# Kernel optimization log

Hardware: AMD Instinct MI355X
Metric: run time of the kernel (lower is better)

## Reference

```python
import jax, jax.numpy as jnp
import numpy as np

B, N, D, H, K, R = 128, 2048, 256, 16, 32, 16
LEAKY_SLOPE = 0.01


def setup_inputs() -> dict:
    key = jax.random.key(0)
    ks = jax.random.split(key, 8)
    s = 0.05
    inp = jax.random.normal(ks[0], (B * N, D), dtype=jnp.float32)
    batch_ids = jnp.repeat(jnp.arange(B, dtype=jnp.int32), N)  # equal-size graphs
    Wk = jax.random.normal(ks[1], (K, D), dtype=jnp.float32) * s
    Wq0 = jax.random.normal(ks[2], (H * K, D), dtype=jnp.float32) * s
    Wq1 = jax.random.normal(ks[3], (H * K, D), dtype=jnp.float32) * s
    We = jax.random.normal(ks[4], (R, D), dtype=jnp.float32) * s
    Wout = jax.random.normal(ks[5], (D, H * R), dtype=jnp.float32) * s
    bout = jax.random.normal(ks[6], (D,), dtype=jnp.float32) * s
    return {"inp": inp, "batch_ids": batch_ids, "Wk": Wk, "Wq0": Wq0,
            "Wq1": Wq1, "We": We, "Wout": Wout, "bout": bout}


def reference(inp, batch_ids, Wk, Wq0, Wq1, We, Wout, bout):
    b = int(jnp.max(batch_ids)) + 1  # number of graphs (static at trace time)
    d = inp.shape[-1]
    # global max pool per graph (torch_geometric global_max_pool)
    pooled = jax.ops.segment_max(inp, batch_ids, num_segments=b)  # [B, D]
    x = inp.reshape(b, -1, d)                                     # [B, N, D]
    keys = jnp.einsum('bnd,kd->bnk', x, Wk)                       # [B, N, K]

    def head_embed(Wq):
        q = (pooled @ Wq.T).reshape(b, H, K)                      # [B, H, K]
        logits = jnp.einsum('bhk,bnk->bhn', q, keys)              # [B, H, N]
        att = jax.nn.softmax(logits, axis=-1)
        feat = jnp.einsum('bhn,bnd->bhd', att, x)                 # [B, H, D]
        return jnp.einsum('bhd,rd->bhr', feat, We)                # [B, H, R]

    dx = (head_embed(Wq0) - head_embed(Wq1)).reshape(b, -1)       # [B, H*R]
    out = dx @ Wout.T + bout
    return jnp.where(out >= 0, out, LEAKY_SLOPE * out)            # LeakyReLU
```

## Files before the change

kernel.cpp:

```cpp
#include <hip/hip_runtime.h>
#include <math.h>

#define B_ 128
#define N_ 2048
#define D_ 256
#define NHEADS 32

#define POOLED_OFF 0
#define P_OFF      32768
#define E_OFF      1081344
#define ML_OFF     5275648
#define FEATP_OFF  5308416

__device__ __forceinline__ void atomic_max_f32(float* addr, float v) {
    if (v >= 0.0f) {
        atomicMax((int*)addr, __float_as_int(v + 0.0f));
    } else {
        atomicMin((unsigned int*)addr, __float_as_uint(v));
    }
}

__device__ __forceinline__ unsigned short f2bf(float f) {
    unsigned u = __float_as_uint(f);
    u += 0x7fff + ((u >> 16) & 1);
    return (unsigned short)(u >> 16);
}
__device__ __forceinline__ float bf2f(unsigned short h) {
    return __uint_as_float(((unsigned)h) << 16);
}

__global__ __launch_bounds__(256) void k_init(float* __restrict__ pooled) {
    pooled[blockIdx.x * 256 + threadIdx.x] = -INFINITY;
}

__global__ __launch_bounds__(256) void k_pool(const float* __restrict__ inp,
                                              float* __restrict__ pooled) {
    int b = blockIdx.x >> 4;
    int ch = blockIdx.x & 15;
    int t = threadIdx.x;
    int sub = t >> 6;
    int dq = (t & 63) * 4;
    const float* p = inp + ((size_t)(b * N_ + ch * 128 + sub)) * D_ + dq;
    float4 m = {-INFINITY, -INFINITY, -INFINITY, -INFINITY};
#pragma unroll 8
    for (int i = 0; i < 32; ++i) {
        float4 v = *(const float4*)(p + (size_t)i * 4 * D_);
        m.x = fmaxf(m.x, v.x); m.y = fmaxf(m.y, v.y);
        m.z = fmaxf(m.z, v.z); m.w = fmaxf(m.w, v.w);
    }
    __shared__ float sm[4 * 256];
    sm[sub * 256 + dq + 0] = m.x;
    sm[sub * 256 + dq + 1] = m.y;
    sm[sub * 256 + dq + 2] = m.z;
    sm[sub * 256 + dq + 3] = m.w;
    __syncthreads();
    float v = fmaxf(fmaxf(sm[t], sm[256 + t]), fmaxf(sm[512 + t], sm[768 + t]));
    atomic_max_f32(pooled + b * D_ + t, v);
}

__global__ __launch_bounds__(256) void k_qp(const float* __restrict__ pooled,
                                            const float* __restrict__ Wq0,
                                            const float* __restrict__ Wq1,
                                            const float* __restrict__ Wk,
                                            float* __restrict__ P) {
    __shared__ float pl[D_];
    __shared__ float ql[1024];
    int b = blockIdx.x, t = threadIdx.x;
    pl[t] = pooled[b * D_ + t];
    __syncthreads();
    for (int rep = 0; rep < 4; ++rep) {
        int idx = rep * 256 + t;
        const float* Wq = (idx < 512) ? Wq0 : Wq1;
        int row = idx & 511;
        const float4* wr = (const float4*)(Wq + (size_t)row * D_);
        float acc = 0.0f;
        for (int dq = 0; dq < 64; ++dq) {
            float4 w = wr[dq];
            const float* pp = &pl[dq * 4];
            acc += w.x * pp[0] + w.y * pp[1] + w.z * pp[2] + w.w * pp[3];
        }
        ql[idx] = acc;
    }
    __syncthreads();
    float wk[32];
#pragma unroll
    for (int k = 0; k < 32; ++k) wk[k] = Wk[k * D_ + t];
    for (int j = 0; j < NHEADS; ++j) {
        const float* q = &ql[(j >> 4) * 512 + (j & 15) * 32];
        float acc = 0.0f;
#pragma unroll
        for (int k = 0; k < 32; ++k) acc = fmaf(q[k], wk[k], acc);
        P[((size_t)b * NHEADS + j) * D_ + t] = acc;
    }
}

__global__ __launch_bounds__(256) void k_logits_e(const float* __restrict__ inp,
                                                  const float* __restrict__ P,
                                                  unsigned short* __restrict__ E,
                                                  float* __restrict__ ml) {
    __shared__ float xs[512 * 20];
    __shared__ float ps[NHEADS * 20];
    int b = blockIdx.x >> 2, nt = blockIdx.x & 3;
    int n0 = nt * 512;
    int t = threadIdx.x;
    int jg = t & 3, ng = t >> 2;
    float acc[8][8] = {};
    const float* xbase = inp + ((size_t)(b * N_ + n0)) * D_;
    const float* pbase = P + (size_t)b * NHEADS * D_;
    for (int c = 0; c < 16; ++c) {
        int d0 = c * 16;
        {
            int q = t & 3, nrow = t >> 2;
            for (int k = 0; k < 8; ++k) {
                int n = nrow + k * 64;
                float4 v = *(const float4*)(xbase + (size_t)n * D_ + d0 + q * 4);
                *(float4*)&xs[n * 20 + q * 4] = v;
            }
            if (t < 128) {
                int j = t >> 2;
                float4 v = *(const float4*)(pbase + (size_t)j * D_ + d0 + q * 4);
                *(float4*)&ps[j * 20 + q * 4] = v;
            }
        }
        __syncthreads();
#pragma unroll
        for (int dd = 0; dd < 16; dd += 4) {
            float4 xa[8], pa[8];
#pragma unroll
            for (int k = 0; k < 8; ++k)
                xa[k] = *(const float4*)&xs[(ng + 64 * k) * 20 + dd];
#pragma unroll
            for (int jj = 0; jj < 8; ++jj)
                pa[jj] = *(const float4*)&ps[(jg + 4 * jj) * 20 + dd];
#pragma unroll
            for (int jj = 0; jj < 8; ++jj)
#pragma unroll
                for (int k = 0; k < 8; ++k)
                    acc[jj][k] += xa[k].x * pa[jj].x + xa[k].y * pa[jj].y +
                                  xa[k].z * pa[jj].z + xa[k].w * pa[jj].w;
        }
        __syncthreads();
    }
    float* red  = xs;
    float* red2 = xs + 2048;
    float* mrow = xs + 2048 + 256;
    int jr = t >> 3, pr = t & 7;
#pragma unroll
    for (int jj = 0; jj < 8; ++jj) {
        float lm = acc[jj][0];
#pragma unroll
        for (int k = 1; k < 8; ++k) lm = fmaxf(lm, acc[jj][k]);
        red[(jg + 4 * jj) * 64 + ng] = lm;
    }
    __syncthreads();
    {
        float v = red[jr * 64 + pr * 8];
#pragma unroll
        for (int i = 1; i < 8; ++i) v = fmaxf(v, red[jr * 64 + pr * 8 + i]);
        red2[jr * 8 + pr] = v;
    }
    __syncthreads();
    if (t < 32) {
        float v = red2[t * 8];
#pragma unroll
        for (int i = 1; i < 8; ++i) v = fmaxf(v, red2[t * 8 + i]);
        mrow[t] = v;
    }
    __syncthreads();
#pragma unroll
    for (int jj = 0; jj < 8; ++jj) {
        int j = jg + 4 * jj;
        float m = mrow[j];
        unsigned short* Eb = E + ((size_t)b * NHEADS + j) * N_ + n0 + ng;
        float s = 0.0f;
#pragma unroll
        for (int k = 0; k < 8; ++k) {
            float e = __expf(acc[jj][k] - m);
            s += e;
            Eb[64 * k] = f2bf(e);
        }
        red[j * 64 + ng] = s;
    }
    __syncthreads();
    {
        float v = 0.0f;
#pragma unroll
        for (int i = 0; i < 8; ++i) v += red[jr * 64 + pr * 8 + i];
        red2[jr * 8 + pr] = v;
    }
    __syncthreads();
    if (t < 32) {
        float v = 0.0f;
#pragma unroll
        for (int i = 0; i < 8; ++i) v += red2[t * 8 + i];
        float* mlp = ml + (((size_t)b * NHEADS + t) * 4 + nt) * 2;
        mlp[0] = mrow[t];
        mlp[1] = v;
    }
}

__global__ __launch_bounds__(256) void k_feat(const float* __restrict__ inp,
                                              const unsigned short* __restrict__ E,
                                              const float* __restrict__ ml,
                                              float* __restrict__ featp) {
    __shared__ float xs[32 * 256];
    __shared__ float as_[32 * 36];
    __shared__ float wcs[32];
    int b = blockIdx.x >> 2, ns = blockIdx.x & 3;
    int n0 = ns * 512;
    int t = threadIdx.x;
    int dg = t & 31, jg = t >> 5;
    if (t < 32) {
        const float* mlb = ml + ((size_t)b * NHEADS + t) * 8;
        float M = fmaxf(fmaxf(mlb[0], mlb[2]), fmaxf(mlb[4], mlb[6]));
        wcs[t] = __expf(mlb[ns * 2] - M);
    }
    float4 accA[4] = {};
    float4 accB[4] = {};
    const float* xb = inp + ((size_t)(b * N_ + n0)) * D_;
    const unsigned short* eb0 = E + (size_t)b * NHEADS * N_ + n0;
    __syncthreads();
    int js = t >> 3, qq = t & 7;
    float wj = wcs[js];
    const unsigned short* ebj = eb0 + (size_t)js * N_ + qq * 4;
    for (int c = 0; c < 16; ++c) {
        {
            int q = t & 63, row = t >> 6;
            for (int k = 0; k < 8; ++k) {
                int n = row + k * 4;
                *(float4*)&xs[n * 256 + q * 4] =
                    *(const float4*)(xb + (size_t)(c * 32 + n) * D_ + q * 4);
            }
            ushort4 ev = *(const ushort4*)(ebj + c * 32);
            float4 av = {bf2f(ev.x) * wj, bf2f(ev.y) * wj,
                         bf2f(ev.z) * wj, bf2f(ev.w) * wj};
            *(float4*)&as_[js * 36 + qq * 4] = av;
        }
        __syncthreads();
#pragma unroll
        for (int nn = 0; nn < 32; nn += 4) {
            float4 aa[4];
#pragma unroll
            for (int jj = 0; jj < 4; ++jj)
                aa[jj] = *(const float4*)&as_[(jg * 4 + jj) * 36 + nn];
#pragma unroll
            for (int i4 = 0; i4 < 4; ++i4) {
                int n = nn + i4;
                float4 xA = *(const float4*)&xs[n * 256 + dg * 4];
                float4 xB = *(const float4*)&xs[n * 256 + 128 + dg * 4];
#pragma unroll
                for (int jj = 0; jj < 4; ++jj) {
                    float a = (i4 == 0) ? aa[jj].x : (i4 == 1) ? aa[jj].y
                            : (i4 == 2) ? aa[jj].z : aa[jj].w;
                    accA[jj].x = fmaf(a, xA.x, accA[jj].x);
                    accA[jj].y = fmaf(a, xA.y, accA[jj].y);
                    accA[jj].z = fmaf(a, xA.z, accA[jj].z);
                    accA[jj].w = fmaf(a, xA.w, accA[jj].w);
                    accB[jj].x = fmaf(a, xB.x, accB[jj].x);
                    accB[jj].y = fmaf(a, xB.y, accB[jj].y);
                    accB[jj].z = fmaf(a, xB.z, accB[jj].z);
                    accB[jj].w = fmaf(a, xB.w, accB[jj].w);
                }
            }
        }
        __syncthreads();
    }
    float* fb = featp + ((size_t)ns * B_ + b) * NHEADS * D_;
#pragma unroll
    for (int jj = 0; jj < 4; ++jj) {
        int j = jg * 4 + jj;
        *(float4*)(fb + (size_t)j * D_ + dg * 4) = accA[jj];
        *(float4*)(fb + (size_t)j * D_ + 128 + dg * 4) = accB[jj];
    }
}

__global__ __launch_bounds__(256) void k_out(const float* __restrict__ featp,
                                             const float* __restrict__ ml,
                                             const float* __restrict__ We,
                                             const float* __restrict__ Wout,
                                             const float* __restrict__ bout,
                                             float* __restrict__ out) {
    __shared__ float f[NHEADS * 257];
    __shared__ float bhrs[512];
    __shared__ float dxs[256];
    __shared__ float linv[NHEADS];
    int b = blockIdx.x, t = threadIdx.x;
    if (t < 32) {
        const float* mlb = ml + ((size_t)b * NHEADS + t) * 8;
        float M = fmaxf(fmaxf(mlb[0], mlb[2]), fmaxf(mlb[4], mlb[6]));
        float L = __expf(mlb[0] - M) * mlb[1] + __expf(mlb[2] - M) * mlb[3] +
                  __expf(mlb[4] - M) * mlb[5] + __expf(mlb[6] - M) * mlb[7];
        linv[t] = 1.0f / L;
    }
    __syncthreads();
    for (int j = 0; j < NHEADS; ++j) {
        float s = 0.0f;
#pragma unroll
        for (int ns = 0; ns < 4; ++ns)
            s += featp[(((size_t)ns * B_ + b) * NHEADS + j) * D_ + t];
        f[j * 257 + t] = s * linv[j];
    }
    __syncthreads();
    for (int rep = 0; rep < 2; ++rep) {
        int idx = rep * 256 + t;
        int j = idx >> 4, r = idx & 15;
        const float* w = We + (size_t)r * D_;
        const float* ff = &f[j * 257];
        float acc = 0.0f;
        for (int d = 0; d < D_; ++d) acc = fmaf(ff[d], w[d], acc);
        bhrs[idx] = acc;
    }
    __syncthreads();
    {
        int h = t >> 4, r = t & 15;
        dxs[t] = bhrs[h * 16 + r] - bhrs[(16 + h) * 16 + r];
    }
    __syncthreads();
    float acc = bout[t];
    const float* wrow = Wout + (size_t)t * 256;
    for (int c = 0; c < 256; ++c) acc = fmaf(dxs[c], wrow[c], acc);
    out[(size_t)b * D_ + t] = acc >= 0.0f ? acc : 0.01f * acc;
}

extern "C" void kernel_launch(void* const* d_in, const int* in_sizes, int n_in,
                              void* d_out, int out_size, void* d_ws, size_t ws_size,
                              hipStream_t stream) {
    const float* inp  = (const float*)d_in[0];
    const float* Wk   = (const float*)d_in[2];
    const float* Wq0  = (const float*)d_in[3];
    const float* Wq1  = (const float*)d_in[4];
    const float* We   = (const float*)d_in[5];
    const float* Wout = (const float*)d_in[6];
    const float* bout = (const float*)d_in[7];
    float* out = (float*)d_out;
    float* ws  = (float*)d_ws;
    float* pooled = ws + POOLED_OFF;
    float* P      = ws + P_OFF;
    unsigned short* E = (unsigned short*)(ws + E_OFF);
    float* ml     = ws + ML_OFF;
    float* featp  = ws + FEATP_OFF;

    k_init<<<dim3(128), dim3(256), 0, stream>>>(pooled);
    k_pool<<<dim3(2048), dim3(256), 0, stream>>>(inp, pooled);
    k_qp<<<dim3(128), dim3(256), 0, stream>>>(pooled, Wq0, Wq1, Wk, P);
    k_logits_e<<<dim3(512), dim3(256), 0, stream>>>(inp, P, E, ml);
    k_feat<<<dim3(512), dim3(256), 0, stream>>>(inp, E, ml, featp);
    k_out<<<dim3(128), dim3(256), 0, stream>>>(featp, ml, We, Wout, bout, out);
}
```

Before: 664.4 us.

## Fuse logits, softmax and feature aggregation into one MFMA kernel with split-bf16 inputs

The pooling kernel now also writes the input as hi/lo bf16 pairs, and the query projection is split the same way. A single fused attention kernel computes logits with three bf16 MFMAs per tile (hi*hi, hi*lo, lo*hi) to approximate fp32. It then does the block-local softmax in registers and aggregates features with bf16 MFMA over an LDS-transposed x tile. This drops the separate E round-trip through global memory and the scalar FMA loops, but adds writes of two bf16 copies of x in the pool pass and lowers the precision of the aggregation step.

```diff
diff --git a/kernel.cpp b/kernel.cpp
--- a/kernel.cpp
+++ b/kernel.cpp
@@ -7,19 +7,26 @@
 #define NHEADS 32
 
 #define POOLED_OFF 0
-#define P_OFF      32768
-#define E_OFF      1081344
-#define ML_OFF     5275648
-#define FEATP_OFF  5308416
+#define PHI_OFF    32768
+#define PLO_OFF    557056
+#define ML_OFF     1081344
+#define FEATP_OFF  1114112
+#define XHI_OFF    5308416
+#define XLO_OFF    38862848
+
+#define XHI_S 0
+#define XLO_S 32768
+#define ATT_S 0
+#define XT_S  33280
+#define STAT_S 53760
+
+typedef __attribute__((ext_vector_type(8))) short short8;
+typedef __attribute__((ext_vector_type(4))) float f32x4;
 
 __device__ __forceinline__ void atomic_max_f32(float* addr, float v) {
-    if (v >= 0.0f) {
-        atomicMax((int*)addr, __float_as_int(v + 0.0f));
-    } else {
-        atomicMin((unsigned int*)addr, __float_as_uint(v));
-    }
-}
-
+    if (v >= 0.0f) atomicMax((int*)addr, __float_as_int(v + 0.0f));
+    else           atomicMin((unsigned int*)addr, __float_as_uint(v));
+}
 __device__ __forceinline__ unsigned short f2bf(float f) {
     unsigned u = __float_as_uint(f);
     u += 0x7fff + ((u >> 16) & 1);
@@ -28,25 +35,39 @@
 __device__ __forceinline__ float bf2f(unsigned short h) {
     return __uint_as_float(((unsigned)h) << 16);
 }
+__device__ __forceinline__ unsigned pack2bf(float a, float b) {
+    return (unsigned)f2bf(a) | ((unsigned)f2bf(b) << 16);
+}
 
 __global__ __launch_bounds__(256) void k_init(float* __restrict__ pooled) {
     pooled[blockIdx.x * 256 + threadIdx.x] = -INFINITY;
 }
 
 __global__ __launch_bounds__(256) void k_pool(const float* __restrict__ inp,
-                                              float* __restrict__ pooled) {
+                                              float* __restrict__ pooled,
+                                              unsigned short* __restrict__ xhi,
+                                              unsigned short* __restrict__ xlo) {
     int b = blockIdx.x >> 4;
     int ch = blockIdx.x & 15;
     int t = threadIdx.x;
     int sub = t >> 6;
     int dq = (t & 63) * 4;
     const float* p = inp + ((size_t)(b * N_ + ch * 128 + sub)) * D_ + dq;
+    size_t nodebase = (size_t)b * N_ + ch * 128 + sub;
     float4 m = {-INFINITY, -INFINITY, -INFINITY, -INFINITY};
-#pragma unroll 8
+#pragma unroll 4
     for (int i = 0; i < 32; ++i) {
         float4 v = *(const float4*)(p + (size_t)i * 4 * D_);
         m.x = fmaxf(m.x, v.x); m.y = fmaxf(m.y, v.y);
         m.z = fmaxf(m.z, v.z); m.w = fmaxf(m.w, v.w);
+        size_t node = nodebase + (size_t)i * 4;
+        ushort4 h4, l4;
+        h4.x = f2bf(v.x); l4.x = f2bf(v.x - bf2f(h4.x));
+        h4.y = f2bf(v.y); l4.y = f2bf(v.y - bf2f(h4.y));
+        h4.z = f2bf(v.z); l4.z = f2bf(v.z - bf2f(h4.z));
+        h4.w = f2bf(v.w); l4.w = f2bf(v.w - bf2f(h4.w));
+        *(ushort4*)(xhi + node * D_ + dq) = h4;
+        *(ushort4*)(xlo + node * D_ + dq) = l4;
     }
     __shared__ float sm[4 * 256];
     sm[sub * 256 + dq + 0] = m.x;
@@ -62,7 +83,8 @@
                                             const float* __restrict__ Wq0,
                                             const float* __restrict__ Wq1,
                                             const float* __restrict__ Wk,
-                                            float* __restrict__ P) {
+                                            unsigned short* __restrict__ Phi,
+                                            unsigned short* __restrict__ Plo) {
     __shared__ float pl[D_];
     __shared__ float ql[1024];
     int b = blockIdx.x, t = threadIdx.x;
@@ -74,9 +96,9 @@
         int row = idx & 511;
         const float4* wr = (const float4*)(Wq + (size_t)row * D_);
         float acc = 0.0f;
-        for (int dq = 0; dq < 64; ++dq) {
-            float4 w = wr[dq];
-            const float* pp = &pl[dq * 4];
+        for (int dqi = 0; dqi < 64; ++dqi) {
+            float4 w = wr[dqi];
+            const float* pp = &pl[dqi * 4];
             acc += w.x * pp[0] + w.y * pp[1] + w.z * pp[2] + w.w * pp[3];
         }
         ql[idx] = acc;
@@ -90,188 +112,173 @@
         float acc = 0.0f;
 #pragma unroll
         for (int k = 0; k < 32; ++k) acc = fmaf(q[k], wk[k], acc);
-        P[((size_t)b * NHEADS + j) * D_ + t] = acc;
-    }
-}
-
-__global__ __launch_bounds__(256) void k_logits_e(const float* __restrict__ inp,
-                                                  const float* __restrict__ P,
-                                                  unsigned short* __restrict__ E,
-                                                  float* __restrict__ ml) {
-    __shared__ float xs[512 * 20];
-    __shared__ float ps[NHEADS * 20];
-    int b = blockIdx.x >> 2, nt = blockIdx.x & 3;
-    int n0 = nt * 512;
+        unsigned short hi = f2bf(acc);
+        unsigned short lo = f2bf(acc - bf2f(hi));
+        Phi[((size_t)b * NHEADS + j) * D_ + t] = hi;
+        Plo[((size_t)b * NHEADS + j) * D_ + t] = lo;
+    }
+}
+
+__global__ __launch_bounds__(256) void k_attn(const unsigned short* __restrict__ xhi,
+                                              const unsigned short* __restrict__ xlo,
+                                              const unsigned short* __restrict__ Phi,
+                                              const unsigned short* __restrict__ Plo,
+                                              float* __restrict__ ml,
+                                              float* __restrict__ featp) {
+    __shared__ uint4 smem4[4096];
+    unsigned char* smem = (unsigned char*)smem4;
+    float* smax = (float*)(smem + STAT_S);
+    float* ssum = (float*)(smem + STAT_S + 512);
+
+    int b = blockIdx.x >> 2, ns = blockIdx.x & 3;
     int t = threadIdx.x;
-    int jg = t & 3, ng = t >> 2;
-    float acc[8][8] = {};
-    const float* xbase = inp + ((size_t)(b * N_ + n0)) * D_;
-    const float* pbase = P + (size_t)b * NHEADS * D_;
+    int w = t >> 6;
+    int lane = t & 63;
+    int lq = lane >> 4;
+    int lm = lane & 15;
+    size_t gnode0 = (size_t)b * N_ + ns * 512;
+
+    f32x4 acc_s[8][2];
+#pragma unroll
+    for (int mt = 0; mt < 8; ++mt)
+#pragma unroll
+        for (int ht = 0; ht < 2; ++ht) acc_s[mt][ht] = (f32x4){0.f, 0.f, 0.f, 0.f};
+
+    int srow = t >> 2, sseg = t & 3;
+    for (int dc = 0; dc < 8; ++dc) {
+        int d0 = dc * 32;
+        short8 bh[2], bl[2];
+#pragma unroll
+        for (int ht = 0; ht < 2; ++ht) {
+            size_t poff = ((size_t)b * NHEADS + ht * 16 + lm) * D_ + d0 + lq * 8;
+            bh[ht] = *(const short8*)(Phi + poff);
+            bl[ht] = *(const short8*)(Plo + poff);
+        }
+        const unsigned short* gxh = xhi + (gnode0 + srow) * D_ + d0 + sseg * 8;
+        const unsigned short* gxl = xlo + (gnode0 + srow) * D_ + d0 + sseg * 8;
+        __syncthreads();
+#pragma unroll
+        for (int i = 0; i < 8; ++i) {
+            *(uint4*)(smem + XHI_S + (size_t)(srow + i * 64) * 64 + sseg * 16) =
+                *(const uint4*)(gxh + (size_t)i * 64 * D_);
+            *(uint4*)(smem + XLO_S + (size_t)(srow + i * 64) * 64 + sseg * 16) =
+                *(const uint4*)(gxl + (size_t)i * 64 * D_);
+        }
+        __syncthreads();
+#pragma unroll
+        for (int mt = 0; mt < 8; ++mt) {
+            size_t roff = (size_t)(w * 128 + mt * 16 + lm) * 64 + lq * 16;
+            short8 ah = *(const short8*)(smem + XHI_S + roff);
+            short8 al = *(const short8*)(smem + XLO_S + roff);
+#pragma unroll
+            for (int ht = 0; ht < 2; ++ht) {
+                acc_s[mt][ht] = __builtin_amdgcn_mfma_f32_16x16x32_bf16(ah, bh[ht], acc_s[mt][ht], 0, 0, 0);
+                acc_s[mt][ht] = __builtin_amdgcn_mfma_f32_16x16x32_bf16(ah, bl[ht], acc_s[mt][ht], 0, 0, 0);
+                acc_s[mt][ht] = __builtin_amdgcn_mfma_f32_16x16x32_bf16(al, bh[ht], acc_s[mt][ht], 0, 0, 0);
+            }
+        }
+    }
+    __syncthreads();
+
+    float bm[2];
+#pragma unroll
+    for (int ht = 0; ht < 2; ++ht) {
+        float m = -INFINITY;
+#pragma unroll
+        for (int mt = 0; mt < 8; ++mt) {
+            m = fmaxf(m, fmaxf(fmaxf(acc_s[mt][ht][0], acc_s[mt][ht][1]),
+                               fmaxf(acc_s[mt][ht][2], acc_s[mt][ht][3])));
+        }
+        m = fmaxf(m, __shfl_xor(m, 16));
+        m = fmaxf(m, __shfl_xor(m, 32));
+        if (lane < 16) smax[w * 32 + ht * 16 + lane] = m;
+    }
+    __syncthreads();
+#pragma unroll
+    for (int ht = 0; ht < 2; ++ht) {
+        bm[ht] = fmaxf(fmaxf(smax[0 * 32 + ht * 16 + lm], smax[1 * 32 + ht * 16 + lm]),
+                       fmaxf(smax[2 * 32 + ht * 16 + lm], smax[3 * 32 + ht * 16 + lm]));
+    }
+#pragma unroll
+    for (int ht = 0; ht < 2; ++ht) {
+        float s = 0.0f;
+#pragma unroll
+        for (int mt = 0; mt < 8; ++mt) {
+            float e0 = __expf(acc_s[mt][ht][0] - bm[ht]);
+            float e1 = __expf(acc_s[mt][ht][1] - bm[ht]);
+            float e2 = __expf(acc_s[mt][ht][2] - bm[ht]);
+            float e3 = __expf(acc_s[mt][ht][3] - bm[ht]);
+            s += (e0 + e1) + (e2 + e3);
+            uint2 pk;
+            pk.x = pack2bf(e0, e1);
+            pk.y = pack2bf(e2, e3);
+            *(uint2*)(smem + ATT_S + (size_t)(ht * 16 + lm) * 1040 +
+                      (size_t)(w * 128 + mt * 16 + lq * 4) * 2) = pk;
+        }
+        s += __shfl_xor(s, 16);
+        s += __shfl_xor(s, 32);
+        if (lane < 16) ssum[w * 32 + ht * 16 + lane] = s;
+    }
+    __syncthreads();
+    if (t < 32) {
+        float mB = fmaxf(fmaxf(smax[t], smax[32 + t]), fmaxf(smax[64 + t], smax[96 + t]));
+        float l = ssum[t] + ssum[32 + t] + ssum[64 + t] + ssum[96 + t];
+        float* mlp = ml + (((size_t)b * NHEADS + t) * 4 + ns) * 2;
+        mlp[0] = mB;
+        mlp[1] = l;
+    }
+    __syncthreads();
+
+    f32x4 acc_o[2][4];
+#pragma unroll
+    for (int mt = 0; mt < 2; ++mt)
+#pragma unroll
+        for (int dt = 0; dt < 4; ++dt) acc_o[mt][dt] = (f32x4){0.f, 0.f, 0.f, 0.f};
+
+    int db = t & 31, nb = t >> 5;
     for (int c = 0; c < 16; ++c) {
-        int d0 = c * 16;
-        {
-            int q = t & 3, nrow = t >> 2;
-            for (int k = 0; k < 8; ++k) {
-                int n = nrow + k * 64;
-                float4 v = *(const float4*)(xbase + (size_t)n * D_ + d0 + q * 4);
-                *(float4*)&xs[n * 20 + q * 4] = v;
-            }
-            if (t < 128) {
-                int j = t >> 2;
-                float4 v = *(const float4*)(pbase + (size_t)j * D_ + d0 + q * 4);
-                *(float4*)&ps[j * 20 + q * 4] = v;
-            }
+        const unsigned short* gx = xhi + (gnode0 + c * 32 + nb * 4) * D_ + db * 8;
+        uint4 R0 = *(const uint4*)(gx);
+        uint4 R1 = *(const uint4*)(gx + D_);
+        uint4 R2 = *(const uint4*)(gx + 2 * D_);
+        uint4 R3 = *(const uint4*)(gx + 3 * D_);
+        const unsigned* r0 = (const unsigned*)&R0;
+        const unsigned* r1 = (const unsigned*)&R1;
+        const unsigned* r2 = (const unsigned*)&R2;
+        const unsigned* r3 = (const unsigned*)&R3;
+        uint2 T[8];
+#pragma unroll
+        for (int c2 = 0; c2 < 4; ++c2) {
+            T[2 * c2 + 0].x = __builtin_amdgcn_perm(r1[c2], r0[c2], 0x05040100u);
+            T[2 * c2 + 0].y = __builtin_amdgcn_perm(r3[c2], r2[c2], 0x05040100u);
+            T[2 * c2 + 1].x = __builtin_amdgcn_perm(r1[c2], r0[c2], 0x07060302u);
+            T[2 * c2 + 1].y = __builtin_amdgcn_perm(r3[c2], r2[c2], 0x07060302u);
         }
         __syncthreads();
 #pragma unroll
-        for (int dd = 0; dd < 16; dd += 4) {
-            float4 xa[8], pa[8];
-#pragma unroll
-            for (int k = 0; k < 8; ++k)
-                xa[k] = *(const float4*)&xs[(ng + 64 * k) * 20 + dd];
-#pragma unroll
-            for (int jj = 0; jj < 8; ++jj)
-                pa[jj] = *(const float4*)&ps[(jg + 4 * jj) * 20 + dd];
-#pragma unroll
-            for (int jj = 0; jj < 8; ++jj)
-#pragma unroll
-                for (int k = 0; k < 8; ++k)
-                    acc[jj][k] += xa[k].x * pa[jj].x + xa[k].y * pa[jj].y +
-                                  xa[k].z * pa[jj].z + xa[k].w * pa[jj].w;
+        for (int j = 0; j < 8; ++j) {
+            int jj = (j + db) & 7;
+            *(uint2*)(smem + XT_S + (size_t)(db * 8 + jj) * 80 + nb * 8) = T[jj];
         }
         __syncthreads();
-    }
-    float* red  = xs;
-    float* red2 = xs + 2048;
-    float* mrow = xs + 2048 + 256;
-    int jr = t >> 3, pr = t & 7;
-#pragma unroll
-    for (int jj = 0; jj < 8; ++jj) {
-        float lm = acc[jj][0];
-#pragma unroll
-        for (int k = 1; k < 8; ++k) lm = fmaxf(lm, acc[jj][k]);
-        red[(jg + 4 * jj) * 64 + ng] = lm;
-    }
-    __syncthreads();
-    {
-        float v = red[jr * 64 + pr * 8];
-#pragma unroll
-        for (int i = 1; i < 8; ++i) v = fmaxf(v, red[jr * 64 + pr * 8 + i]);
-        red2[jr * 8 + pr] = v;
-    }
-    __syncthreads();
-    if (t < 32) {
-        float v = red2[t * 8];
-#pragma unroll
-        for (int i = 1; i < 8; ++i) v = fmaxf(v, red2[t * 8 + i]);
-        mrow[t] = v;
-    }
-    __syncthreads();
-#pragma unroll
-    for (int jj = 0; jj < 8; ++jj) {
-        int j = jg + 4 * jj;
-        float m = mrow[j];
-        unsigned short* Eb = E + ((size_t)b * NHEADS + j) * N_ + n0 + ng;
-        float s = 0.0f;
-#pragma unroll
-        for (int k = 0; k < 8; ++k) {
-            float e = __expf(acc[jj][k] - m);
-            s += e;
-            Eb[64 * k] = f2bf(e);
-        }
-        red[j * 64 + ng] = s;
-    }
-    __syncthreads();
-    {
-        float v = 0.0f;
-#pragma unroll
-        for (int i = 0; i < 8; ++i) v += red[jr * 64 + pr * 8 + i];
-        red2[jr * 8 + pr] = v;
-    }
-    __syncthreads();
-    if (t < 32) {
-        float v = 0.0f;
-#pragma unroll
-        for (int i = 0; i < 8; ++i) v += red2[t * 8 + i];
-        float* mlp = ml + (((size_t)b * NHEADS + t) * 4 + nt) * 2;
-        mlp[0] = mrow[t];
-        mlp[1] = v;
-    }
-}
-
-__global__ __launch_bounds__(256) void k_feat(const float* __restrict__ inp,
-                                              const unsigned short* __restrict__ E,
-                                              const float* __restrict__ ml,
-                                              float* __restrict__ featp) {
-    __shared__ float xs[32 * 256];
-    __shared__ float as_[32 * 36];
-    __shared__ float wcs[32];
-    int b = blockIdx.x >> 2, ns = blockIdx.x & 3;
-    int n0 = ns * 512;
-    int t = threadIdx.x;
-    int dg = t & 31, jg = t >> 5;
-    if (t < 32) {
-        const float* mlb = ml + ((size_t)b * NHEADS + t) * 8;
-        float M = fmaxf(fmaxf(mlb[0], mlb[2]), fmaxf(mlb[4], mlb[6]));
-        wcs[t] = __expf(mlb[ns * 2] - M);
-    }
-    float4 accA[4] = {};
-    float4 accB[4] = {};
-    const float* xb = inp + ((size_t)(b * N_ + n0)) * D_;
-    const unsigned short* eb0 = E + (size_t)b * NHEADS * N_ + n0;
-    __syncthreads();
-    int js = t >> 3, qq = t & 7;
-    float wj = wcs[js];
-    const unsigned short* ebj = eb0 + (size_t)js * N_ + qq * 4;
-    for (int c = 0; c < 16; ++c) {
-        {
-            int q = t & 63, row = t >> 6;
-            for (int k = 0; k < 8; ++k) {
-                int n = row + k * 4;
-                *(float4*)&xs[n * 256 + q * 4] =
-                    *(const float4*)(xb + (size_t)(c * 32 + n) * D_ + q * 4);
-            }
-            ushort4 ev = *(const ushort4*)(ebj + c * 32);
-            float4 av = {bf2f(ev.x) * wj, bf2f(ev.y) * wj,
-                         bf2f(ev.z) * wj, bf2f(ev.w) * wj};
-            *(float4*)&as_[js * 36 + qq * 4] = av;
-        }
-        __syncthreads();
-#pragma unroll
-        for (int nn = 0; nn < 32; nn += 4) {
-            float4 aa[4];
-#pragma unroll
-            for (int jj = 0; jj < 4; ++jj)
-                aa[jj] = *(const float4*)&as_[(jg * 4 + jj) * 36 + nn];
-#pragma unroll
-            for (int i4 = 0; i4 < 4; ++i4) {
-                int n = nn + i4;
-                float4 xA = *(const float4*)&xs[n * 256 + dg * 4];
-                float4 xB = *(const float4*)&xs[n * 256 + 128 + dg * 4];
-#pragma unroll
-                for (int jj = 0; jj < 4; ++jj) {
-                    float a = (i4 == 0) ? aa[jj].x : (i4 == 1) ? aa[jj].y
-                            : (i4 == 2) ? aa[jj].z : aa[jj].w;
-                    accA[jj].x = fmaf(a, xA.x, accA[jj].x);
-                    accA[jj].y = fmaf(a, xA.y, accA[jj].y);
-                    accA[jj].z = fmaf(a, xA.z, accA[jj].z);
-                    accA[jj].w = fmaf(a, xA.w, accA[jj].w);
-                    accB[jj].x = fmaf(a, xB.x, accB[jj].x);
-                    accB[jj].y = fmaf(a, xB.y, accB[jj].y);
-                    accB[jj].z = fmaf(a, xB.z, accB[jj].z);
-                    accB[jj].w = fmaf(a, xB.w, accB[jj].w);
-                }
-            }
-        }
-        __syncthreads();
-    }
-    float* fb = featp + ((size_t)ns * B_ + b) * NHEADS * D_;
-#pragma unroll
-    for (int jj = 0; jj < 4; ++jj) {
-        int j = jg * 4 + jj;
-        *(float4*)(fb + (size_t)j * D_ + dg * 4) = accA[jj];
-        *(float4*)(fb + (size_t)j * D_ + 128 + dg * 4) = accB[jj];
-    }
+        short8 a0 = *(const short8*)(smem + ATT_S + (size_t)lm * 1040 + (size_t)(c * 32 + lq * 8) * 2);
+        short8 a1 = *(const short8*)(smem + ATT_S + (size_t)(16 + lm) * 1040 + (size_t)(c * 32 + lq * 8) * 2);
+#pragma unroll
+        for (int dt = 0; dt < 4; ++dt) {
+            short8 bf = *(const short8*)(smem + XT_S + (size_t)(w * 64 + dt * 16 + lm) * 80 + lq * 16);
+            acc_o[0][dt] = __builtin_amdgcn_mfma_f32_16x16x32_bf16(a0, bf, acc_o[0][dt], 0, 0, 0);
+            acc_o[1][dt] = __builtin_amdgcn_mfma_f32_16x16x32_bf16(a1, bf, acc_o[1][dt], 0, 0, 0);
+        }
+    }
+    float* fb = featp + ((size_t)(ns * B_ + b)) * D_ * NHEADS;
+#pragma unroll
+    for (int mt = 0; mt < 2; ++mt)
+#pragma unroll
+        for (int dt = 0; dt < 4; ++dt) {
+            int d = w * 64 + dt * 16 + lm;
+            int h0 = mt * 16 + lq * 4;
+            *(f32x4*)(fb + (size_t)d * NHEADS + h0) = acc_o[mt][dt];
+        }
 }
 
 __global__ __launch_bounds__(256) void k_out(const float* __restrict__ featp,
@@ -283,31 +290,45 @@
     __shared__ float f[NHEADS * 257];
     __shared__ float bhrs[512];
     __shared__ float dxs[256];
-    __shared__ float linv[NHEADS];
+    __shared__ float wns[4 * 32];
+    __shared__ float linv2[32];
     int b = blockIdx.x, t = threadIdx.x;
     if (t < 32) {
         const float* mlb = ml + ((size_t)b * NHEADS + t) * 8;
         float M = fmaxf(fmaxf(mlb[0], mlb[2]), fmaxf(mlb[4], mlb[6]));
-        float L = __expf(mlb[0] - M) * mlb[1] + __expf(mlb[2] - M) * mlb[3] +
-                  __expf(mlb[4] - M) * mlb[5] + __expf(mlb[6] - M) * mlb[7];
-        linv[t] = 1.0f / L;
-    }
-    __syncthreads();
-    for (int j = 0; j < NHEADS; ++j) {
-        float s = 0.0f;
-#pragma unroll
-        for (int ns = 0; ns < 4; ++ns)
-            s += featp[(((size_t)ns * B_ + b) * NHEADS + j) * D_ + t];
-        f[j * 257 + t] = s * linv[j];
-    }
+        float e0 = __expf(mlb[0] - M), e1 = __expf(mlb[2] - M);
+        float e2 = __expf(mlb[4] - M), e3 = __expf(mlb[6] - M);
+        float L = e0 * mlb[1] + e1 * mlb[3] + e2 * mlb[5] + e3 * mlb[7];
+        wns[0 * 32 + t] = e0; wns[1 * 32 + t] = e1;
+        wns[2 * 32 + t] = e2; wns[3 * 32 + t] = e3;
+        linv2[t] = 1.0f / L;
+    }
+    __syncthreads();
+    float fj[32];
+#pragma unroll
+    for (int j = 0; j < 32; ++j) fj[j] = 0.0f;
+#pragma unroll
+    for (int ns = 0; ns < 4; ++ns) {
+        const float* fp = featp + ((size_t)(ns * B_ + b) * D_ + t) * NHEADS;
+#pragma unroll
+        for (int j4 = 0; j4 < 8; ++j4) {
+            float4 v = *(const float4*)(fp + j4 * 4);
+            fj[j4 * 4 + 0] += wns[ns * 32 + j4 * 4 + 0] * v.x;
+            fj[j4 * 4 + 1] += wns[ns * 32 + j4 * 4 + 1] * v.y;
+            fj[j4 * 4 + 2] += wns[ns * 32 + j4 * 4 + 2] * v.z;
+            fj[j4 * 4 + 3] += wns[ns * 32 + j4 * 4 + 3] * v.w;
+        }
+    }
+#pragma unroll
+    for (int j = 0; j < 32; ++j) f[j * 257 + t] = fj[j] * linv2[j];
     __syncthreads();
     for (int rep = 0; rep < 2; ++rep) {
         int idx = rep * 256 + t;
         int j = idx >> 4, r = idx & 15;
-        const float* w = We + (size_t)r * D_;
+        const float* wrow = We + (size_t)r * D_;
         const float* ff = &f[j * 257];
         float acc = 0.0f;
-        for (int d = 0; d < D_; ++d) acc = fmaf(ff[d], w[d], acc);
+        for (int d = 0; d < D_; ++d) acc = fmaf(ff[d], wrow[d], acc);
         bhrs[idx] = acc;
     }
     __syncthreads();
@@ -335,15 +356,16 @@
     float* out = (float*)d_out;
     float* ws  = (float*)d_ws;
     float* pooled = ws + POOLED_OFF;
-    float* P      = ws + P_OFF;
-    unsigned short* E = (unsigned short*)(ws + E_OFF);
+    unsigned short* Phi = (unsigned short*)(ws + PHI_OFF);
+    unsigned short* Plo = (unsigned short*)(ws + PLO_OFF);
     float* ml     = ws + ML_OFF;
     float* featp  = ws + FEATP_OFF;
+    unsigned short* xhi = (unsigned short*)(ws + XHI_OFF);
+    unsigned short* xlo = (unsigned short*)(ws + XLO_OFF);
 
     k_init<<<dim3(128), dim3(256), 0, stream>>>(pooled);
-    k_pool<<<dim3(2048), dim3(256), 0, stream>>>(inp, pooled);
-    k_qp<<<dim3(128), dim3(256), 0, stream>>>(pooled, Wq0, Wq1, Wk, P);
-    k_logits_e<<<dim3(512), dim3(256), 0, stream>>>(inp, P, E, ml);
-    k_feat<<<dim3(512), dim3(256), 0, stream>>>(inp, E, ml, featp);
+    k_pool<<<dim3(2048), dim3(256), 0, stream>>>(inp, pooled, xhi, xlo);
+    k_qp<<<dim3(128), dim3(256), 0, stream>>>(pooled, Wq0, Wq1, Wk, Phi, Plo);
+    k_attn<<<dim3(512), dim3(256), 0, stream>>>(xhi, xlo, Phi, Plo, ml, featp);
     k_out<<<dim3(128), dim3(256), 0, stream>>>(featp, ml, We, Wout, bout, out);
 }
```

Measured after the change: 609.4 us. 1.09x faster.
